# Optimization experiments

Measured on AMD Instinct MI355X. Metric: run time of the kernel, lower is better.

## Reference

```python
import jax, jax.numpy as jnp
import numpy as np

NUM_HEADS = 12

def setup_inputs() -> dict:
    key = jax.random.key(0)
    ks = jax.random.split(key, 6)
    B, N, C = 16, 1024, 768
    H, d = NUM_HEADS, C // NUM_HEADS
    return {
        "x": jax.random.normal(ks[0], (B, N, C), dtype=jnp.float32),
        "W_qkv": jax.random.normal(ks[1], (C, 3 * C), dtype=jnp.float32) * 0.02,
        "b_qkv": jax.random.normal(ks[2], (3 * C,), dtype=jnp.float32) * 0.02,
        "zeta": jnp.ones((1, 1, H, 1, d), dtype=jnp.float32),
        "W_proj": jax.random.normal(ks[3], (C, C), dtype=jnp.float32) * 0.02,
        "b_proj": jax.random.normal(ks[4], (C,), dtype=jnp.float32) * 0.02,
        "mask": jnp.zeros((B, N), dtype=bool),
    }

def reference(x, W_qkv, b_qkv, zeta, W_proj, b_proj, mask):
    B, N, C = x.shape
    H = NUM_HEADS
    d = C // H
    scale = d ** -0.5
    # qkv: (B,N,3C) -> (B,N,3,H,d) -> (3,B,H,N,d), gated by zeta (1,1,H,1,d)
    qkv = (x @ W_qkv + b_qkv).reshape(B, N, 3, H, d).transpose(2, 0, 3, 1, 4)
    qkv = qkv * zeta
    q, k, v = qkv[0], qkv[1], qkv[2]
    attn = jnp.einsum("bhnd,bhmd->bhnm", q, k) * scale
    # mask (B,N) over keys -> (B,1,1,N)
    attn = jnp.where(mask[:, None, None, :], -jnp.inf, attn)
    attn = jax.nn.softmax(attn, axis=-1)
    out = jnp.einsum("bhnm,bhmd->bhnd", attn, v)          # (B,H,N,d)
    out = out.transpose(0, 2, 1, 3).reshape(B, N, C)
    return out @ W_proj + b_proj
```

## Files before the change

### kernel.cpp

```cpp
#include <hip/hip_runtime.h>
#include <hip/hip_bf16.h>

typedef unsigned short ushort_t;
typedef __bf16 bf16_t;
typedef bf16_t bf16x8 __attribute__((ext_vector_type(8)));
typedef float floatx4 __attribute__((ext_vector_type(4)));
typedef ushort_t ushortx8 __attribute__((ext_vector_type(8)));

struct alignas(8) us4 { ushort_t x, y, z, w; };

__device__ __forceinline__ ushort_t f2bf(float f) {
  union { float f; unsigned int u; } v; v.f = f;
  unsigned int u = v.u;
  return (ushort_t)((u + 0x7fffu + ((u >> 16) & 1u)) >> 16);
}

__device__ __forceinline__ unsigned int pk_bf16(float a, float b) {
  __hip_bfloat162 h = __float22bfloat162_rn(float2{a, b});
  union { __hip_bfloat162 h; unsigned int u; } v; v.h = h;
  return v.u;
}

__device__ __forceinline__ void async16(const void* g, void* l) {
  __builtin_amdgcn_global_load_lds(
      (const __attribute__((address_space(1))) unsigned int*)g,
      (__attribute__((address_space(3))) unsigned int*)l, 16, 0, 0);
}

#define LOG2E 1.44269504088896340736f


__global__ __launch_bounds__(256) void k_prep(const float* __restrict__ x,
                                              ushort_t* __restrict__ xb,
                                              const float* __restrict__ Wq,
                                              ushort_t* __restrict__ WqT,
                                              const float* __restrict__ Wp,
                                              ushort_t* __restrict__ WpT) {
  __shared__ float tile[32][33];
  const int bid = blockIdx.x, t = threadIdx.x;
  if (bid < 6144) {
    size_t i = ((size_t)bid * 256 + t) * 8;
    float4 a = *(const float4*)(x + i);
    float4 b = *(const float4*)(x + i + 4);
    ushortx8 o;
    o[0] = f2bf(a.x); o[1] = f2bf(a.y); o[2] = f2bf(a.z); o[3] = f2bf(a.w);
    o[4] = f2bf(b.x); o[5] = f2bf(b.y); o[6] = f2bf(b.z); o[7] = f2bf(b.w);
    *(ushortx8*)(xb + i) = o;
    return;
  }
  const float* in; ushort_t* out; int C, c0, r0;
  if (bid < 7872) {
    int b2 = bid - 6144;
    in = Wq; out = WqT; C = 2304;
    c0 = (b2 % 72) * 32; r0 = (b2 / 72) * 32;
  } else {
    int b3 = bid - 7872;
    in = Wp; out = WpT; C = 768;
    c0 = (b3 % 24) * 32; r0 = (b3 / 24) * 32;
  }
  const int tx = t & 31, ty = t >> 5;
#pragma unroll
  for (int i = 0; i < 32; i += 8)
    tile[ty + i][tx] = in[(size_t)(r0 + ty + i) * C + c0 + tx];
  __syncthreads();
#pragma unroll
  for (int i = 0; i < 32; i += 8)
    out[(size_t)(c0 + ty + i) * 768 + r0 + tx] = f2bf(tile[tx][ty + i]);
}


__device__ __forceinline__ void gemm_pipe3(const ushort_t* __restrict__ A,
                                           const ushort_t* __restrict__ Bt,
                                           int m0, int n0,
                                           ushort_t* sA, ushort_t* sB,
                                           floatx4 acc[4][4]) {
  const int t = threadIdx.x;
  const int lane = t & 63, w = t >> 6;
  const int wr = w >> 1, wc = w & 1;
  const int lr = lane & 15, qd = lane >> 4;
  const int swz = ((t & 3) ^ ((t >> 3) & 3)) * 8;
  const ushort_t* gA = A + (size_t)(m0 + (t >> 2)) * 768 + swz;
  const ushort_t* gB = Bt + (size_t)(n0 + (t >> 2)) * 768 + swz;
  char* lA = (char*)sA + t * 16;
  char* lB = (char*)sB + t * 16;
  const int rsz = (qd ^ ((lr >> 1) & 3)) * 16;
#define ISSUE(kk, buf)                                    \
  do {                                                    \
    const int k0_ = (kk) * 32, b_ = (buf) * 8192;         \
    async16(gA + k0_, lA + b_);                           \
    async16(gA + k0_ + 64 * 768, lA + b_ + 4096);         \
    async16(gB + k0_, lB + b_);                           \
    async16(gB + k0_ + 64 * 768, lB + b_ + 4096);         \
  } while (0)
  ISSUE(0, 0);
  ISSUE(1, 1);
  asm volatile("s_waitcnt vmcnt(4)" ::: "memory");
  asm volatile("s_barrier" ::: "memory");
#pragma unroll
  for (int k = 0; k < 24; ++k) {
    if (k + 2 < 24) ISSUE(k + 2, (k + 2) % 3);
    const char* cA = (const char*)sA + (k % 3) * 8192;
    const char* cB = (const char*)sB + (k % 3) * 8192;
    bf16x8 af[4], bfr[4];
#pragma unroll
    for (int i = 0; i < 4; ++i)
      af[i] = *(const bf16x8*)(cA + (wr * 64 + i * 16 + lr) * 64 + rsz);
#pragma unroll
    for (int j = 0; j < 4; ++j)
      bfr[j] = *(const bf16x8*)(cB + (wc * 64 + j * 16 + lr) * 64 + rsz);
#pragma unroll
    for (int i = 0; i < 4; ++i)
#pragma unroll
      for (int j = 0; j < 4; ++j)
        acc[i][j] = __builtin_amdgcn_mfma_f32_16x16x32_bf16(af[i], bfr[j], acc[i][j], 0, 0, 0);
    if (k < 22)
      asm volatile("s_waitcnt vmcnt(4)" ::: "memory");
    else if (k == 22)
      asm volatile("s_waitcnt vmcnt(0)" ::: "memory");
    if (k < 23) asm volatile("s_barrier" ::: "memory");
  }
#undef ISSUE
}


__global__ __launch_bounds__(256, 3) void k_qkv(const ushort_t* __restrict__ xb,
                                                const ushort_t* __restrict__ WqT,
                                                const float* __restrict__ bqkv,
                                                const float* __restrict__ zeta,
                                                ushort_t* __restrict__ qb,
                                                ushort_t* __restrict__ kb,
                                                ushort_t* __restrict__ vtb) {
  __shared__ alignas(16) ushort_t sA[3 * 4096];
  __shared__ alignas(16) ushort_t sB[3 * 4096];
  floatx4 acc[4][4] = {};
  const int lin = blockIdx.x;
  const int xcd = lin & 7, idx = lin >> 3;
  const int m0 = (xcd * 16 + (idx & 15)) * 128;
  const int n0 = (idx >> 4) * 128;
  gemm_pipe3(xb, WqT, m0, n0, sA, sB, acc);
  const int t = threadIdx.x, lane = t & 63, w = t >> 6;
  const int wr = w >> 1, wc = w & 1, lr = lane & 15, qd = lane >> 4;
  const int tq = n0 / 768;
#pragma unroll
  for (int j = 0; j < 4; ++j) {
    int n = n0 + wc * 64 + j * 16 + lr;
    int nc = n - tq * 768;
    int h = nc >> 6, dim = n & 63;
    float bias = bqkv[n];
    float zv = zeta[nc];
    float mult = (tq == 0) ? zv * 0.125f * LOG2E : zv;
    if (tq < 2) {
      ushort_t* dst = (tq == 0) ? qb : kb;
#pragma unroll
      for (int i = 0; i < 4; ++i) {
        int mbase = m0 + wr * 64 + i * 16 + qd * 4;
#pragma unroll
        for (int r = 0; r < 4; ++r) {
          int m = mbase + r;
          int b = m >> 10, seq = m & 1023;
          dst[(((size_t)b * 12 + h) * 1024 + seq) * 64 + dim] = f2bf((acc[i][j][r] + bias) * mult);
        }
      }
    } else {
#pragma unroll
      for (int i = 0; i < 4; ++i) {
        int mbase = m0 + wr * 64 + i * 16 + qd * 4;
        int b = mbase >> 10, seq = mbase & 1023;
        us4 pk;
        pk.x = f2bf((acc[i][j][0] + bias) * mult);
        pk.y = f2bf((acc[i][j][1] + bias) * mult);
        pk.z = f2bf((acc[i][j][2] + bias) * mult);
        pk.w = f2bf((acc[i][j][3] + bias) * mult);
        *(us4*)&vtb[(((size_t)b * 12 + h) * 64 + dim) * 1024 + seq] = pk;
      }
    }
  }
}


__global__ __launch_bounds__(256, 3) void k_attn(const ushort_t* __restrict__ qg,
                                                 const ushort_t* __restrict__ kg,
                                                 const ushort_t* __restrict__ vg,
                                                 const unsigned char* __restrict__ mask,
                                                 ushort_t* __restrict__ ob) {
  __shared__ alignas(16) char smem[49664];
  char* sV = smem + 32768;
  float* maskadd = (float*)(smem + 49152);
  const int t = threadIdx.x, lane = t & 63, w = t >> 6;
  const int lr = lane & 15, qd = lane >> 4;
  const int lin = blockIdx.x;
  const int bh = (lin & 7) + 8 * (lin >> 6);
  const int qt = (lin >> 3) & 7;
  const int b = bh / 12, h = bh % 12;
  const int qrow0 = qt * 128 + w * 32;
  const ushort_t* qp = qg + (size_t)bh * 65536;
  const ushort_t* kp = kg + (size_t)bh * 65536;
  const ushort_t* vp = vg + (size_t)bh * 65536;
  const unsigned char* mp = mask + b * 1024;

  bf16x8 qf[2][2];
#pragma unroll
  for (int ns = 0; ns < 2; ++ns)
#pragma unroll
    for (int kk = 0; kk < 2; ++kk)
      qf[ns][kk] = *(const bf16x8*)(qp + (size_t)(qrow0 + ns * 16 + lr) * 64 + kk * 32 + qd * 8);

  floatx4 o[4][2] = {};
  float lst[2] = {0.f, 0.f};
  char* sPw = smem + 16384 + w * 4096;

  for (int kt = 0; kt < 8; ++kt) {
    __syncthreads();
    const ushort_t* kpt = kp + kt * 8192;
#pragma unroll
    for (int it = 0; it < 4; ++it) {
      int p = it * 256 + t;
      int r = p >> 3, cs = (p & 7) ^ (r & 7);
      async16(kpt + r * 64 + cs * 8, smem + p * 16);
    }
    const ushort_t* vpt = vp + kt * 128;
#pragma unroll
    for (int it = 0; it < 4; ++it) {
      int p = it * 256 + t;
      int r = p >> 4, cs = (p & 15) ^ (r & 15);
      async16(vpt + (size_t)r * 1024 + cs * 8, sV + p * 16);
    }
    if (t < 128) maskadd[t] = mp[kt * 128 + t] ? -1e30f : 0.0f;
    asm volatile("s_waitcnt vmcnt(0)" ::: "memory");
    __syncthreads();

#pragma unroll
    for (int hh = 0; hh < 2; ++hh) {
      floatx4 s[4][2] = {};
#pragma unroll
      for (int kk = 0; kk < 2; ++kk) {
#pragma unroll
        for (int ms = 0; ms < 4; ++ms) {
          bf16x8 ak = *(const bf16x8*)(smem + ((hh * 4 + ms) * 16 + lr) * 128 +
                                       ((kk * 4 + qd) ^ (lr & 7)) * 16);
#pragma unroll
          for (int ns = 0; ns < 2; ++ns)
            s[ms][ns] = __builtin_amdgcn_mfma_f32_16x16x32_bf16(ak, qf[ns][kk], s[ms][ns], 0, 0, 0);
        }
      }
#pragma unroll
      for (int ms = 0; ms < 4; ++ms) {
        float4 mk = *(const float4*)&maskadd[(hh * 4 + ms) * 16 + qd * 4];
#pragma unroll
        for (int ns = 0; ns < 2; ++ns) {
          float p0 = __builtin_amdgcn_exp2f(s[ms][ns][0] + mk.x);
          float p1 = __builtin_amdgcn_exp2f(s[ms][ns][1] + mk.y);
          float p2 = __builtin_amdgcn_exp2f(s[ms][ns][2] + mk.z);
          float p3 = __builtin_amdgcn_exp2f(s[ms][ns][3] + mk.w);
          lst[ns] += (p0 + p1) + (p2 + p3);
          uint2 pk;
          pk.x = pk_bf16(p0, p1);
          pk.y = pk_bf16(p2, p3);
          *(uint2*)(sPw + (ns * 16 + lr) * 128 +
                    ((ms * 2 + (qd >> 1)) ^ (lr & 7)) * 16 + (qd & 1) * 8) = pk;
        }
      }
      asm volatile("s_waitcnt lgkmcnt(0)" ::: "memory");
#pragma unroll
      for (int kk = 0; kk < 2; ++kk) {
        bf16x8 pb[2];
#pragma unroll
        for (int ns = 0; ns < 2; ++ns)
          pb[ns] = *(const bf16x8*)(sPw + (ns * 16 + lr) * 128 +
                                    ((kk * 4 + qd) ^ (lr & 7)) * 16);
#pragma unroll
        for (int ds = 0; ds < 4; ++ds) {
          bf16x8 av = *(const bf16x8*)(sV + (ds * 16 + lr) * 256 +
                                       ((hh * 8 + kk * 4 + qd) ^ lr) * 16);
#pragma unroll
          for (int ns = 0; ns < 2; ++ns)
            o[ds][ns] = __builtin_amdgcn_mfma_f32_16x16x32_bf16(av, pb[ns], o[ds][ns], 0, 0, 0);
        }
      }
    }
  }
#pragma unroll
  for (int ns = 0; ns < 2; ++ns) {
    lst[ns] += __shfl_xor(lst[ns], 16);
    lst[ns] += __shfl_xor(lst[ns], 32);
  }
#pragma unroll
  for (int ns = 0; ns < 2; ++ns) {
    float rl = 1.0f / lst[ns];
    size_t row = (size_t)(b * 1024 + qrow0 + ns * 16 + lr) * 768 + h * 64;
#pragma unroll
    for (int ds = 0; ds < 4; ++ds) {
      uint2 ov;
      ov.x = pk_bf16(o[ds][ns][0] * rl, o[ds][ns][1] * rl);
      ov.y = pk_bf16(o[ds][ns][2] * rl, o[ds][ns][3] * rl);
      *(uint2*)&ob[row + ds * 16 + qd * 4] = ov;
    }
  }
}


__global__ __launch_bounds__(256, 3) void k_proj(const ushort_t* __restrict__ ob,
                                                 const ushort_t* __restrict__ WpT,
                                                 const float* __restrict__ bproj,
                                                 float* __restrict__ out) {
  __shared__ alignas(16) ushort_t sA[3 * 4096];
  __shared__ alignas(16) ushort_t sB[3 * 4096];
  floatx4 acc[4][4] = {};
  const int lin = blockIdx.x;
  const int xcd = lin & 7, idx = lin >> 3;
  const int m0 = (xcd * 16 + (idx & 15)) * 128;
  const int n0 = (idx >> 4) * 128;
  gemm_pipe3(ob, WpT, m0, n0, sA, sB, acc);
  const int t = threadIdx.x, lane = t & 63, w = t >> 6;
  const int wr = w >> 1, wc = w & 1, lr = lane & 15, qd = lane >> 4;
#pragma unroll
  for (int j = 0; j < 4; ++j) {
    int n = n0 + wc * 64 + j * 16 + lr;
    float bias = bproj[n];
#pragma unroll
    for (int i = 0; i < 4; ++i) {
      int mbase = m0 + wr * 64 + i * 16 + qd * 4;
#pragma unroll
      for (int r = 0; r < 4; ++r)
        out[(size_t)(mbase + r) * 768 + n] = acc[i][j][r] + bias;
    }
  }
}


extern "C" void kernel_launch(void* const* d_in, const int* in_sizes, int n_in,
                              void* d_out, int out_size, void* d_ws, size_t ws_size,
                              hipStream_t stream) {
  const float* x = (const float*)d_in[0];
  const float* bqkv = (const float*)d_in[2];
  const float* zeta = (const float*)d_in[3];
  const float* bproj = (const float*)d_in[5];
  const unsigned char* mask = (const unsigned char*)d_in[6];
  float* out = (float*)d_out;
  char* ws = (char*)d_ws;
  ushort_t* xb  = (ushort_t*)(ws);
  ushort_t* WqT = (ushort_t*)(ws + 25165824);
  ushort_t* WpT = (ushort_t*)(ws + 28704768);
  ushort_t* qb  = (ushort_t*)(ws + 29884416);
  ushort_t* kb  = (ushort_t*)(ws + 55050240);
  ushort_t* vtb = (ushort_t*)(ws + 80216064);
  ushort_t* ob  = xb;

  k_prep<<<dim3(8448), dim3(256), 0, stream>>>(x, xb, (const float*)d_in[1], WqT,
                                               (const float*)d_in[4], WpT);
  k_qkv<<<dim3(2304), dim3(256), 0, stream>>>(xb, WqT, bqkv, zeta, qb, kb, vtb);
  k_attn<<<dim3(1536), dim3(256), 0, stream>>>(qb, kb, vtb, mask, ob);
  k_proj<<<dim3(768), dim3(256), 0, stream>>>(ob, WpT, bproj, out);
}
```

Measured before the change: 290.5 us.

## Shrink LDS footprints to raise occupancy: double-buffer GEMMs, halve attention P buffer

The GEMM mainloop drops from a 3-stage to a 2-stage async pipeline, cutting shared memory per block from 48KB to 32KB, and launch bounds are raised to 4 blocks per CU. The attention kernel halves its per-wave P staging buffer by writing and consuming P in two k-chunks. It also replaces the shared-memory float mask with mask bytes loaded into registers and applied by select after exp2. The aim is more resident blocks for latency hiding, at the cost of a shallower prefetch that waits on every load each k-step, and tighter register limits that could cause spills.

```diff
diff --git a/kernel.cpp b/kernel.cpp
--- a/kernel.cpp
+++ b/kernel.cpp
@@ -69,7 +69,7 @@
 }
 
 
-__device__ __forceinline__ void gemm_pipe3(const ushort_t* __restrict__ A,
+__device__ __forceinline__ void gemm_pipe2(const ushort_t* __restrict__ A,
                                            const ushort_t* __restrict__ Bt,
                                            int m0, int n0,
                                            ushort_t* sA, ushort_t* sB,
@@ -93,14 +93,13 @@
     async16(gB + k0_ + 64 * 768, lB + b_ + 4096);         \
   } while (0)
   ISSUE(0, 0);
-  ISSUE(1, 1);
-  asm volatile("s_waitcnt vmcnt(4)" ::: "memory");
+  asm volatile("s_waitcnt vmcnt(0)" ::: "memory");
   asm volatile("s_barrier" ::: "memory");
 #pragma unroll
   for (int k = 0; k < 24; ++k) {
-    if (k + 2 < 24) ISSUE(k + 2, (k + 2) % 3);
-    const char* cA = (const char*)sA + (k % 3) * 8192;
-    const char* cB = (const char*)sB + (k % 3) * 8192;
+    if (k + 1 < 24) ISSUE(k + 1, (k + 1) & 1);
+    const char* cA = (const char*)sA + (k & 1) * 8192;
+    const char* cB = (const char*)sB + (k & 1) * 8192;
     bf16x8 af[4], bfr[4];
 #pragma unroll
     for (int i = 0; i < 4; ++i)
@@ -113,31 +112,30 @@
 #pragma unroll
       for (int j = 0; j < 4; ++j)
         acc[i][j] = __builtin_amdgcn_mfma_f32_16x16x32_bf16(af[i], bfr[j], acc[i][j], 0, 0, 0);
-    if (k < 22)
-      asm volatile("s_waitcnt vmcnt(4)" ::: "memory");
-    else if (k == 22)
+    if (k + 1 < 24) {
       asm volatile("s_waitcnt vmcnt(0)" ::: "memory");
-    if (k < 23) asm volatile("s_barrier" ::: "memory");
+      asm volatile("s_barrier" ::: "memory");
+    }
   }
 #undef ISSUE
 }
 
 
-__global__ __launch_bounds__(256, 3) void k_qkv(const ushort_t* __restrict__ xb,
+__global__ __launch_bounds__(256, 4) void k_qkv(const ushort_t* __restrict__ xb,
                                                 const ushort_t* __restrict__ WqT,
                                                 const float* __restrict__ bqkv,
                                                 const float* __restrict__ zeta,
                                                 ushort_t* __restrict__ qb,
                                                 ushort_t* __restrict__ kb,
                                                 ushort_t* __restrict__ vtb) {
-  __shared__ alignas(16) ushort_t sA[3 * 4096];
-  __shared__ alignas(16) ushort_t sB[3 * 4096];
+  __shared__ alignas(16) ushort_t sA[2 * 4096];
+  __shared__ alignas(16) ushort_t sB[2 * 4096];
   floatx4 acc[4][4] = {};
   const int lin = blockIdx.x;
   const int xcd = lin & 7, idx = lin >> 3;
   const int m0 = (xcd * 16 + (idx & 15)) * 128;
   const int n0 = (idx >> 4) * 128;
-  gemm_pipe3(xb, WqT, m0, n0, sA, sB, acc);
+  gemm_pipe2(xb, WqT, m0, n0, sA, sB, acc);
   const int t = threadIdx.x, lane = t & 63, w = t >> 6;
   const int wr = w >> 1, wc = w & 1, lr = lane & 15, qd = lane >> 4;
   const int tq = n0 / 768;
@@ -178,14 +176,13 @@
 }
 
 
-__global__ __launch_bounds__(256, 3) void k_attn(const ushort_t* __restrict__ qg,
+__global__ __launch_bounds__(256, 4) void k_attn(const ushort_t* __restrict__ qg,
                                                  const ushort_t* __restrict__ kg,
                                                  const ushort_t* __restrict__ vg,
                                                  const unsigned char* __restrict__ mask,
                                                  ushort_t* __restrict__ ob) {
-  __shared__ alignas(16) char smem[49664];
-  char* sV = smem + 32768;
-  float* maskadd = (float*)(smem + 49152);
+  __shared__ alignas(16) char smem[40960];
+  char* sV = smem + 24576;
   const int t = threadIdx.x, lane = t & 63, w = t >> 6;
   const int lr = lane & 15, qd = lane >> 4;
   const int lin = blockIdx.x;
@@ -207,7 +204,7 @@
 
   floatx4 o[4][2] = {};
   float lst[2] = {0.f, 0.f};
-  char* sPw = smem + 16384 + w * 4096;
+  char* sPw = smem + 16384 + w * 2048;
 
   for (int kt = 0; kt < 8; ++kt) {
     __syncthreads();
@@ -225,7 +222,12 @@
       int r = p >> 4, cs = (p & 15) ^ (r & 15);
       async16(vpt + (size_t)r * 1024 + cs * 8, sV + p * 16);
     }
-    if (t < 128) maskadd[t] = mp[kt * 128 + t] ? -1e30f : 0.0f;
+    unsigned int mw[2][4];
+#pragma unroll
+    for (int mh = 0; mh < 2; ++mh)
+#pragma unroll
+      for (int ms = 0; ms < 4; ++ms)
+        mw[mh][ms] = *(const unsigned int*)(mp + kt * 128 + (mh * 4 + ms) * 16 + qd * 4);
     asm volatile("s_waitcnt vmcnt(0)" ::: "memory");
     __syncthreads();
 
@@ -244,30 +246,34 @@
         }
       }
 #pragma unroll
-      for (int ms = 0; ms < 4; ++ms) {
-        float4 mk = *(const float4*)&maskadd[(hh * 4 + ms) * 16 + qd * 4];
-#pragma unroll
-        for (int ns = 0; ns < 2; ++ns) {
-          float p0 = __builtin_amdgcn_exp2f(s[ms][ns][0] + mk.x);
-          float p1 = __builtin_amdgcn_exp2f(s[ms][ns][1] + mk.y);
-          float p2 = __builtin_amdgcn_exp2f(s[ms][ns][2] + mk.z);
-          float p3 = __builtin_amdgcn_exp2f(s[ms][ns][3] + mk.w);
-          lst[ns] += (p0 + p1) + (p2 + p3);
-          uint2 pk;
-          pk.x = pk_bf16(p0, p1);
-          pk.y = pk_bf16(p2, p3);
-          *(uint2*)(sPw + (ns * 16 + lr) * 128 +
-                    ((ms * 2 + (qd >> 1)) ^ (lr & 7)) * 16 + (qd & 1) * 8) = pk;
+      for (int kk = 0; kk < 2; ++kk) {
+#pragma unroll
+        for (int ms2 = 0; ms2 < 2; ++ms2) {
+          const int ms = kk * 2 + ms2;
+          const unsigned int m4 = mw[hh][ms];
+#pragma unroll
+          for (int ns = 0; ns < 2; ++ns) {
+            float p0 = __builtin_amdgcn_exp2f(s[ms][ns][0]);
+            float p1 = __builtin_amdgcn_exp2f(s[ms][ns][1]);
+            float p2 = __builtin_amdgcn_exp2f(s[ms][ns][2]);
+            float p3 = __builtin_amdgcn_exp2f(s[ms][ns][3]);
+            p0 = (m4 & 0x000000ffu) ? 0.f : p0;
+            p1 = (m4 & 0x0000ff00u) ? 0.f : p1;
+            p2 = (m4 & 0x00ff0000u) ? 0.f : p2;
+            p3 = (m4 & 0xff000000u) ? 0.f : p3;
+            lst[ns] += (p0 + p1) + (p2 + p3);
+            uint2 pk;
+            pk.x = pk_bf16(p0, p1);
+            pk.y = pk_bf16(p2, p3);
+            *(uint2*)(sPw + (ms2 * 2 + (qd >> 1)) * 512 +
+                      (ns * 16 + lr) * 16 + (qd & 1) * 8) = pk;
+          }
         }
-      }
-      asm volatile("s_waitcnt lgkmcnt(0)" ::: "memory");
-#pragma unroll
-      for (int kk = 0; kk < 2; ++kk) {
+        asm volatile("s_waitcnt lgkmcnt(0)" ::: "memory");
         bf16x8 pb[2];
 #pragma unroll
         for (int ns = 0; ns < 2; ++ns)
-          pb[ns] = *(const bf16x8*)(sPw + (ns * 16 + lr) * 128 +
-                                    ((kk * 4 + qd) ^ (lr & 7)) * 16);
+          pb[ns] = *(const bf16x8*)(sPw + qd * 512 + (ns * 16 + lr) * 16);
 #pragma unroll
         for (int ds = 0; ds < 4; ++ds) {
           bf16x8 av = *(const bf16x8*)(sV + (ds * 16 + lr) * 256 +
@@ -299,18 +305,18 @@
 }
 
 
-__global__ __launch_bounds__(256, 3) void k_proj(const ushort_t* __restrict__ ob,
+__global__ __launch_bounds__(256, 4) void k_proj(const ushort_t* __restrict__ ob,
                                                  const ushort_t* __restrict__ WpT,
                                                  const float* __restrict__ bproj,
                                                  float* __restrict__ out) {
-  __shared__ alignas(16) ushort_t sA[3 * 4096];
-  __shared__ alignas(16) ushort_t sB[3 * 4096];
+  __shared__ alignas(16) ushort_t sA[2 * 4096];
+  __shared__ alignas(16) ushort_t sB[2 * 4096];
   floatx4 acc[4][4] = {};
   const int lin = blockIdx.x;
   const int xcd = lin & 7, idx = lin >> 3;
   const int m0 = (xcd * 16 + (idx & 15)) * 128;
   const int n0 = (idx >> 4) * 128;
-  gemm_pipe3(ob, WpT, m0, n0, sA, sB, acc);
+  gemm_pipe2(ob, WpT, m0, n0, sA, sB, acc);
   const int t = threadIdx.x, lane = t & 63, w = t >> 6;
   const int wr = w >> 1, wc = w & 1, lr = lane & 15, qd = lane >> 4;
 #pragma unroll
```

After: 309.8 us. +6.7%, slower.
